# Performance work log

Measured on AMD Instinct MI355X. Metric: run time of the kernel, lower is better.

Reference implementation:

```python
import jax, jax.numpy as jnp
import numpy as np

B, I, H = 4096, 2048, 2048


def setup_inputs() -> dict:
    key = jax.random.key(0)
    k1, k2, k3, k4, k5 = jax.random.split(key, 5)
    return {
        "x": jax.random.normal(k1, (B, I), dtype=jnp.float32),
        "coefficients": jax.random.normal(k2, (I, H), dtype=jnp.float32) * 0.1,
        "amplitude_an": jax.random.normal(k3, (1, I, H), dtype=jnp.float32) * 0.1,
        "amplitude_bn": jax.random.normal(k4, (1, I, H), dtype=jnp.float32) * 0.1,
        "bias": jax.random.normal(k5, (1, I), dtype=jnp.float32),
    }


def reference(x, coefficients, amplitude_an, amplitude_bn, bias):
    # phase[b,h] = x[b,:] @ coefficients[:,h]  (same matmul done per-sample in torch loop)
    phase = x @ coefficients  # [B, H]
    num_harmonics = coefficients.shape[1]
    # sum over harmonics of an[i,h]*cos(phase[b,h]) + bn[i,h]*sin(phase[b,h])
    gain = (
        jnp.einsum("bh,ih->bi", jnp.cos(phase), amplitude_an[0])
        + jnp.einsum("bh,ih->bi", jnp.sin(phase), amplitude_bn[0])
        + num_harmonics * bias  # bias added per-harmonic before the sum over H
    )
    return gain  # [B, I]
```

## Files before the change

kernel.cpp:

```cpp
#include <hip/hip_runtime.h>
#include <hip/hip_bf16.h>

#define B_DIM 4096
#define I_DIM 2048
#define H_DIM 2048

typedef unsigned char u8;
typedef unsigned short u16;
typedef unsigned int u32;
typedef __attribute__((ext_vector_type(4))) float f32x4;
typedef __attribute__((ext_vector_type(4))) int i32x4;
typedef __attribute__((ext_vector_type(8))) int i32x8;

#define SBAR __builtin_amdgcn_sched_barrier(0)

__device__ __forceinline__ void gload_lds16(const void* g, void* l) {
  __builtin_amdgcn_global_load_lds(
      (const __attribute__((address_space(1))) void*)g,
      (__attribute__((address_space(3))) void*)l, 16, 0, 0);
}

__device__ __forceinline__ u32 f2fp4(float v, float inv_scale) {
  const float a = fabsf(v) * inv_scale;
  u32 m = (u32)(a > 0.25f) + (u32)(a > 0.75f) + (u32)(a > 1.25f) +
          (u32)(a > 1.75f) + (u32)(a > 2.5f) + (u32)(a > 3.5f) + (u32)(a > 5.0f);
  return ((__float_as_uint(v) >> 31) << 3) | m;
}

__global__ void prep_all(const float* __restrict__ x, const float* __restrict__ coeff,
                         const float* __restrict__ an, const float* __restrict__ bn,
                         u16* __restrict__ xf4, u16* __restrict__ ct4,
                         u32* __restrict__ ab4) {
  if (blockIdx.x < 4096) {
    __shared__ float tile[32][33];
    const int h0 = (blockIdx.x & 63) * 32;
    const int i0 = (blockIdx.x >> 6) * 32;
    const int tid = threadIdx.x;
    const int tx = tid & 31;
    const int ty = tid >> 5;
    for (int r = ty; r < 32; r += 8)
      tile[r][tx] = coeff[(long)(i0 + r) * H_DIM + (h0 + tx)];
    __syncthreads();
    const int hl = tid >> 3;
    const int q = (tid & 7) * 4;
    u32 w = f2fp4(tile[q + 0][hl], 8.f) | (f2fp4(tile[q + 1][hl], 8.f) << 4) |
            (f2fp4(tile[q + 2][hl], 8.f) << 8) | (f2fp4(tile[q + 3][hl], 8.f) << 12);
    ct4[(long)(h0 + hl) * (I_DIM / 4) + ((i0 + q) >> 2)] = (u16)w;
    return;
  }
  const long NX4 = (long)B_DIM * I_DIM / 4;
  const long NA4 = (long)I_DIM * H_DIM / 4;
  const long total = NX4 + NA4;
  const long stride = (long)1024 * blockDim.x;
  for (long t = (long)(blockIdx.x - 4096) * blockDim.x + threadIdx.x; t < total;
       t += stride) {
    if (t < NX4) {
      float4 v = *(const float4*)(x + t * 4);
      u32 b0 = f2fp4(v.x, 1.f) | (f2fp4(v.y, 1.f) << 4);
      u32 b1 = f2fp4(v.z, 1.f) | (f2fp4(v.w, 1.f) << 4);
      xf4[t] = (u16)(b0 | (b1 << 8));
    } else {
      long p = (t - NX4) * 4;
      float4 va = *(const float4*)(an + p);
      float4 vb = *(const float4*)(bn + p);
      u32 b0 = f2fp4(va.x, 8.f) | (f2fp4(vb.x, 8.f) << 4);
      u32 b1 = f2fp4(va.y, 8.f) | (f2fp4(vb.y, 8.f) << 4);
      u32 b2 = f2fp4(va.z, 8.f) | (f2fp4(vb.z, 8.f) << 4);
      u32 b3 = f2fp4(va.w, 8.f) | (f2fp4(vb.w, 8.f) << 4);
      ab4[p >> 2] = b0 | (b1 << 8) | (b2 << 16) | (b3 << 24);
    }
  }
}

#define NBUF 49152

__device__ __forceinline__ void stageA1(const char* Ab, long kbyte, long lda,
                                        char* buf, int tid, int i) {
  const int o = i * 8192 + tid * 16;
  const int row = o >> 7;
  const int ls = ((((o >> 4) & 7) ^ (row & 7)) << 4);
  gload_lds16(Ab + (long)row * lda + kbyte + ls, buf + o);
}
__device__ __forceinline__ void stageB1(const char* Bb, long kbyte, long ldb,
                                        char* buf, int tid, int i) {
  const int o = i * 8192 + tid * 16;
  const int row = o >> 7;
  const int ls = ((((o >> 4) & 7) ^ (row & 7)) << 4);
  gload_lds16(Bb + (long)row * ldb + kbyte + ls, buf + 16384 + o);
}

__device__ __forceinline__ i32x4 frag_ld16(const char* S, int row, int slot) {
  return *(const i32x4*)(S + row * 128 + ((slot ^ (row & 7)) << 4));
}

template <int SA, int SB>
__device__ __forceinline__ void gemm_kloop_fp4(const char* __restrict__ A,
                                               const char* __restrict__ Bt,
                                               int rowA0, int colB0, long Kbytes,
                                               char* smem, f32x4 acc[4][4]) {
  const int tid = threadIdx.x;
  const int lane = tid & 63;
  const int wid = tid >> 6;
  const int wr = wid >> 2;
  const int wc = wid & 3;
  const long lda = Kbytes, ldb = Kbytes;
  const char* Ab = A + (long)rowA0 * lda;
  const char* Bb = Bt + (long)colB0 * ldb;
  const int arow = wr * 64 + (lane & 15);
  const int brow = wc * 64 + (lane & 15);
  const int g = lane >> 4;
  const int nt = (int)(Kbytes >> 7);

  char* b0 = smem;
  char* b1 = smem + NBUF;
  char* b2 = smem + 2 * NBUF;

#pragma unroll
  for (int i = 0; i < 2; ++i) stageA1(Ab, 0, lda, b0, tid, i);
#pragma unroll
  for (int i = 0; i < 4; ++i) stageB1(Bb, 0, ldb, b0, tid, i);
#pragma unroll
  for (int i = 0; i < 2; ++i) stageA1(Ab, 128, lda, b1, tid, i);
#pragma unroll
  for (int i = 0; i < 4; ++i) stageB1(Bb, 128, ldb, b1, tid, i);

  for (int t = 0; t < nt; ++t) {
    if (t < nt - 1) asm volatile("s_waitcnt vmcnt(6)" ::: "memory");
    else            asm volatile("s_waitcnt vmcnt(0)" ::: "memory");
    SBAR;
    __builtin_amdgcn_s_barrier();
    SBAR;

    const bool st = (t + 2 < nt);
    const long kb2 = (long)(t + 2) * 128;
    i32x8 af[2][4], bfr[2][4];

#pragma unroll
    for (int m = 0; m < 4; ++m)
      *(i32x4*)&af[0][m] = frag_ld16(b0, arow + m * 16, g);
    *(i32x4*)&bfr[0][0] = frag_ld16(b0 + 16384, brow, g);
    *(i32x4*)&bfr[0][1] = frag_ld16(b0 + 16384, brow + 16, g);
    if (st) { stageA1(Ab, kb2, lda, b2, tid, 0); stageA1(Ab, kb2, lda, b2, tid, 1); }
    SBAR;
    asm volatile("s_waitcnt lgkmcnt(0)" ::: "memory");
    SBAR;
    __builtin_amdgcn_s_setprio(1);
#pragma unroll
    for (int m = 0; m < 4; ++m)
#pragma unroll
      for (int n = 0; n < 2; ++n)
        acc[m][n] = __builtin_amdgcn_mfma_scale_f32_16x16x128_f8f6f4(
            af[0][m], bfr[0][n], acc[m][n], 4, 4, 0, SA, 0, SB);
    __builtin_amdgcn_s_setprio(0);
    SBAR;
    __builtin_amdgcn_s_barrier();

#pragma unroll
    for (int m = 0; m < 4; ++m)
      *(i32x4*)&af[1][m] = frag_ld16(b0, arow + m * 16, 4 + g);
    *(i32x4*)&bfr[0][2] = frag_ld16(b0 + 16384, brow + 32, g);
    *(i32x4*)&bfr[0][3] = frag_ld16(b0 + 16384, brow + 48, g);
    if (st) { stageB1(Bb, kb2, ldb, b2, tid, 0); stageB1(Bb, kb2, ldb, b2, tid, 1); }
    SBAR;
    asm volatile("s_waitcnt lgkmcnt(0)" ::: "memory");
    SBAR;
    __builtin_amdgcn_s_setprio(1);
#pragma unroll
    for (int m = 0; m < 4; ++m)
#pragma unroll
      for (int n = 2; n < 4; ++n)
        acc[m][n] = __builtin_amdgcn_mfma_scale_f32_16x16x128_f8f6f4(
            af[0][m], bfr[0][n], acc[m][n], 4, 4, 0, SA, 0, SB);
    __builtin_amdgcn_s_setprio(0);
    SBAR;
    __builtin_amdgcn_s_barrier();

    *(i32x4*)&bfr[1][0] = frag_ld16(b0 + 16384, brow, 4 + g);
    *(i32x4*)&bfr[1][1] = frag_ld16(b0 + 16384, brow + 16, 4 + g);
    if (st) stageB1(Bb, kb2, ldb, b2, tid, 2);
    SBAR;
    asm volatile("s_waitcnt lgkmcnt(0)" ::: "memory");
    SBAR;
    __builtin_amdgcn_s_setprio(1);
#pragma unroll
    for (int m = 0; m < 4; ++m)
#pragma unroll
      for (int n = 0; n < 2; ++n)
        acc[m][n] = __builtin_amdgcn_mfma_scale_f32_16x16x128_f8f6f4(
            af[1][m], bfr[1][n], acc[m][n], 4, 4, 0, SA, 0, SB);
    __builtin_amdgcn_s_setprio(0);
    SBAR;
    __builtin_amdgcn_s_barrier();

    *(i32x4*)&bfr[1][2] = frag_ld16(b0 + 16384, brow + 32, 4 + g);
    *(i32x4*)&bfr[1][3] = frag_ld16(b0 + 16384, brow + 48, 4 + g);
    if (st) stageB1(Bb, kb2, ldb, b2, tid, 3);
    SBAR;
    asm volatile("s_waitcnt lgkmcnt(0)" ::: "memory");
    SBAR;
    __builtin_amdgcn_s_setprio(1);
#pragma unroll
    for (int m = 0; m < 4; ++m)
#pragma unroll
      for (int n = 2; n < 4; ++n)
        acc[m][n] = __builtin_amdgcn_mfma_scale_f32_16x16x128_f8f6f4(
            af[1][m], bfr[1][n], acc[m][n], 4, 4, 0, SA, 0, SB);
    __builtin_amdgcn_s_setprio(0);
    SBAR;

    char* tmp = b0; b0 = b1; b1 = b2; b2 = tmp;
  }
}

__device__ __forceinline__ void tile_xy(int& bx, int& by) {
  const int bid = blockIdx.x;
  const int xcd = bid & 7;
  const int loc = bid >> 3;
  bx = (xcd & 1) * 4 + (loc & 3);
  by = (xcd >> 1) * 8 + (loc >> 2);
}

__global__ __launch_bounds__(512, 1) void gemm_phase(const char* __restrict__ xf4,
                                                     const char* __restrict__ ct4,
                                                     u8* __restrict__ cs4) {
  __shared__ __align__(16) char smem[3 * NBUF];
  int bx, by;
  tile_xy(bx, by);
  const int rowA0 = by * 128;
  const int colB0 = bx * 256;
  f32x4 acc[4][4];
#pragma unroll
  for (int m = 0; m < 4; ++m)
#pragma unroll
    for (int n = 0; n < 4; ++n)
#pragma unroll
      for (int j = 0; j < 4; ++j) acc[m][n][j] = 0.0f;

  gemm_kloop_fp4<0x7F7F7F7F, 0x7C7C7C7C>(xf4, ct4, rowA0, colB0, I_DIM / 2, smem, acc);

  const int lane = threadIdx.x & 63;
  const int wid = threadIdx.x >> 6;
  const int wr = wid >> 2, wc = wid & 3;
#pragma unroll
  for (int m = 0; m < 4; ++m) {
#pragma unroll
    for (int n = 0; n < 4; ++n) {
      const int col = colB0 + wc * 64 + n * 16 + (lane & 15);
#pragma unroll
      for (int j = 0; j < 4; ++j) {
        const int row = rowA0 + wr * 64 + m * 16 + (lane >> 4) * 4 + j;
        const float p = acc[m][n][j];
        const u32 b = f2fp4(__cosf(p), 4.f) | (f2fp4(__sinf(p), 4.f) << 4);
        cs4[(long)row * H_DIM + col] = (u8)b;
      }
    }
  }
}

__global__ __launch_bounds__(512, 1) void gemm_gain(const char* __restrict__ cs4,
                                                    const char* __restrict__ ab4,
                                                    const float* __restrict__ bias,
                                                    float* __restrict__ out) {
  __shared__ __align__(16) char smem[3 * NBUF];
  int bx, by;
  tile_xy(bx, by);
  const int rowA0 = by * 128;
  const int colB0 = bx * 256;
  f32x4 acc[4][4];
#pragma unroll
  for (int m = 0; m < 4; ++m)
#pragma unroll
    for (int n = 0; n < 4; ++n)
#pragma unroll
      for (int j = 0; j < 4; ++j) acc[m][n][j] = 0.0f;

  gemm_kloop_fp4<0x7D7D7D7D, 0x7C7C7C7C>(cs4, ab4, rowA0, colB0, H_DIM, smem, acc);

  const int lane = threadIdx.x & 63;
  const int wid = threadIdx.x >> 6;
  const int wr = wid >> 2, wc = wid & 3;
#pragma unroll
  for (int m = 0; m < 4; ++m) {
#pragma unroll
    for (int n = 0; n < 4; ++n) {
      const int col = colB0 + wc * 64 + n * 16 + (lane & 15);
      const float bv = 2048.0f * bias[col];
#pragma unroll
      for (int j = 0; j < 4; ++j) {
        const int row = rowA0 + wr * 64 + m * 16 + (lane >> 4) * 4 + j;
        out[(long)row * I_DIM + col] = acc[m][n][j] + bv;
      }
    }
  }
}

extern "C" void kernel_launch(void* const* d_in, const int* in_sizes, int n_in,
                              void* d_out, int out_size, void* d_ws, size_t ws_size,
                              hipStream_t stream) {
  const float* x     = (const float*)d_in[0];
  const float* coeff = (const float*)d_in[1];
  const float* an    = (const float*)d_in[2];
  const float* bn    = (const float*)d_in[3];
  const float* bias  = (const float*)d_in[4];
  float* out = (float*)d_out;

  char* ws = (char*)d_ws;
  char* xf4 = ws;
  char* ct4 = ws + (4L << 20);
  char* ab4 = ws + (8L << 20);
  u8*  cs4  = (u8*)(ws + (12L << 20));

  prep_all<<<5120, 256, 0, stream>>>(x, coeff, an, bn, (u16*)xf4, (u16*)ct4,
                                     (u32*)ab4);
  gemm_phase<<<256, 512, 0, stream>>>(xf4, ct4, cs4);
  gemm_gain<<<256, 512, 0, stream>>>((const char*)cs4, (const char*)ab4, bias, out);
}
```

Before: 67.69 us.

## Reschedule FP4 GEMM k-loop with partial LDS waits and fewer barriers

The GEMM k-loop is reordered so more LDS fragment reads are issued ahead of the MFMA groups. Full lgkmcnt(0) waits become partial waits, and three intra-iteration workgroup barriers are removed, keeping only the per-iteration barrier that guards the triple buffer. Separately, the coefficient-transpose part of prep makes each block handle 8 tiles, which cuts the grid from 5120 to 1536 blocks. The phase epilogue uses a single __sincosf call, and both GEMMs declare launch_bounds(512,2). The tighter register limit may cause spills, and with about 147KB of LDS per block only one block can fit per CU anyway; the partial lgkmcnt counts also assume a particular instruction ordering.

```diff
diff --git a/kernel.cpp b/kernel.cpp
--- a/kernel.cpp
+++ b/kernel.cpp
@@ -13,6 +13,7 @@
 typedef __attribute__((ext_vector_type(8))) int i32x8;
 
 #define SBAR __builtin_amdgcn_sched_barrier(0)
+#define NBUF 49152
 
 __device__ __forceinline__ void gload_lds16(const void* g, void* l) {
   __builtin_amdgcn_global_load_lds(
@@ -31,28 +32,33 @@
                          const float* __restrict__ an, const float* __restrict__ bn,
                          u16* __restrict__ xf4, u16* __restrict__ ct4,
                          u32* __restrict__ ab4) {
-  if (blockIdx.x < 4096) {
+  if (blockIdx.x < 512) {
     __shared__ float tile[32][33];
-    const int h0 = (blockIdx.x & 63) * 32;
-    const int i0 = (blockIdx.x >> 6) * 32;
     const int tid = threadIdx.x;
     const int tx = tid & 31;
     const int ty = tid >> 5;
-    for (int r = ty; r < 32; r += 8)
-      tile[r][tx] = coeff[(long)(i0 + r) * H_DIM + (h0 + tx)];
-    __syncthreads();
     const int hl = tid >> 3;
     const int q = (tid & 7) * 4;
-    u32 w = f2fp4(tile[q + 0][hl], 8.f) | (f2fp4(tile[q + 1][hl], 8.f) << 4) |
-            (f2fp4(tile[q + 2][hl], 8.f) << 8) | (f2fp4(tile[q + 3][hl], 8.f) << 12);
-    ct4[(long)(h0 + hl) * (I_DIM / 4) + ((i0 + q) >> 2)] = (u16)w;
+#pragma unroll
+    for (int rep = 0; rep < 8; ++rep) {
+      const int tidx = blockIdx.x * 8 + rep;
+      const int h0 = (tidx & 63) * 32;
+      const int i0 = (tidx >> 6) * 32;
+      for (int r = ty; r < 32; r += 8)
+        tile[r][tx] = coeff[(long)(i0 + r) * H_DIM + (h0 + tx)];
+      __syncthreads();
+      u32 w = f2fp4(tile[q + 0][hl], 8.f) | (f2fp4(tile[q + 1][hl], 8.f) << 4) |
+              (f2fp4(tile[q + 2][hl], 8.f) << 8) | (f2fp4(tile[q + 3][hl], 8.f) << 12);
+      ct4[(long)(h0 + hl) * (I_DIM / 4) + ((i0 + q) >> 2)] = (u16)w;
+      __syncthreads();
+    }
     return;
   }
   const long NX4 = (long)B_DIM * I_DIM / 4;
   const long NA4 = (long)I_DIM * H_DIM / 4;
   const long total = NX4 + NA4;
   const long stride = (long)1024 * blockDim.x;
-  for (long t = (long)(blockIdx.x - 4096) * blockDim.x + threadIdx.x; t < total;
+  for (long t = (long)(blockIdx.x - 512) * blockDim.x + threadIdx.x; t < total;
        t += stride) {
     if (t < NX4) {
       float4 v = *(const float4*)(x + t * 4);
@@ -72,21 +78,25 @@
   }
 }
 
-#define NBUF 49152
-
-__device__ __forceinline__ void stageA1(const char* Ab, long kbyte, long lda,
-                                        char* buf, int tid, int i) {
-  const int o = i * 8192 + tid * 16;
-  const int row = o >> 7;
-  const int ls = ((((o >> 4) & 7) ^ (row & 7)) << 4);
-  gload_lds16(Ab + (long)row * lda + kbyte + ls, buf + o);
-}
-__device__ __forceinline__ void stageB1(const char* Bb, long kbyte, long ldb,
-                                        char* buf, int tid, int i) {
-  const int o = i * 8192 + tid * 16;
-  const int row = o >> 7;
-  const int ls = ((((o >> 4) & 7) ^ (row & 7)) << 4);
-  gload_lds16(Bb + (long)row * ldb + kbyte + ls, buf + 16384 + o);
+__device__ __forceinline__ void stageA2(const char* Ab, long kbyte, long lda,
+                                        char* buf, int tid) {
+#pragma unroll
+  for (int i = 0; i < 2; ++i) {
+    const int o = i * 8192 + tid * 16;
+    const int row = o >> 7;
+    const int ls = ((((o >> 4) & 7) ^ (row & 7)) << 4);
+    gload_lds16(Ab + (long)row * lda + kbyte + ls, buf + o);
+  }
+}
+__device__ __forceinline__ void stageB2(const char* Bb, long kbyte, long ldb,
+                                        char* buf, int tid, int i0) {
+#pragma unroll
+  for (int i = 0; i < 2; ++i) {
+    const int o = (i0 + i) * 8192 + tid * 16;
+    const int row = o >> 7;
+    const int ls = ((((o >> 4) & 7) ^ (row & 7)) << 4);
+    gload_lds16(Bb + (long)row * ldb + kbyte + ls, buf + 16384 + o);
+  }
 }
 
 __device__ __forceinline__ i32x4 frag_ld16(const char* S, int row, int slot) {
@@ -115,14 +125,10 @@
   char* b1 = smem + NBUF;
   char* b2 = smem + 2 * NBUF;
 
-#pragma unroll
-  for (int i = 0; i < 2; ++i) stageA1(Ab, 0, lda, b0, tid, i);
-#pragma unroll
-  for (int i = 0; i < 4; ++i) stageB1(Bb, 0, ldb, b0, tid, i);
-#pragma unroll
-  for (int i = 0; i < 2; ++i) stageA1(Ab, 128, lda, b1, tid, i);
-#pragma unroll
-  for (int i = 0; i < 4; ++i) stageB1(Bb, 128, ldb, b1, tid, i);
+  stageA2(Ab, 0, lda, b0, tid);   stageB2(Bb, 0, ldb, b0, tid, 0);
+  stageB2(Bb, 0, ldb, b0, tid, 2);
+  stageA2(Ab, 128, lda, b1, tid); stageB2(Bb, 128, ldb, b1, tid, 0);
+  stageB2(Bb, 128, ldb, b1, tid, 2);
 
   for (int t = 0; t < nt; ++t) {
     if (t < nt - 1) asm volatile("s_waitcnt vmcnt(6)" ::: "memory");
@@ -140,9 +146,12 @@
       *(i32x4*)&af[0][m] = frag_ld16(b0, arow + m * 16, g);
     *(i32x4*)&bfr[0][0] = frag_ld16(b0 + 16384, brow, g);
     *(i32x4*)&bfr[0][1] = frag_ld16(b0 + 16384, brow + 16, g);
-    if (st) { stageA1(Ab, kb2, lda, b2, tid, 0); stageA1(Ab, kb2, lda, b2, tid, 1); }
-    SBAR;
-    asm volatile("s_waitcnt lgkmcnt(0)" ::: "memory");
+    if (st) stageA2(Ab, kb2, lda, b2, tid);
+    SBAR;
+    *(i32x4*)&bfr[0][2] = frag_ld16(b0 + 16384, brow + 32, g);
+    *(i32x4*)&bfr[0][3] = frag_ld16(b0 + 16384, brow + 48, g);
+    SBAR;
+    asm volatile("s_waitcnt lgkmcnt(2)" ::: "memory");
     SBAR;
     __builtin_amdgcn_s_setprio(1);
 #pragma unroll
@@ -153,16 +162,15 @@
             af[0][m], bfr[0][n], acc[m][n], 4, 4, 0, SA, 0, SB);
     __builtin_amdgcn_s_setprio(0);
     SBAR;
-    __builtin_amdgcn_s_barrier();
 
 #pragma unroll
     for (int m = 0; m < 4; ++m)
       *(i32x4*)&af[1][m] = frag_ld16(b0, arow + m * 16, 4 + g);
-    *(i32x4*)&bfr[0][2] = frag_ld16(b0 + 16384, brow + 32, g);
-    *(i32x4*)&bfr[0][3] = frag_ld16(b0 + 16384, brow + 48, g);
-    if (st) { stageB1(Bb, kb2, ldb, b2, tid, 0); stageB1(Bb, kb2, ldb, b2, tid, 1); }
-    SBAR;
-    asm volatile("s_waitcnt lgkmcnt(0)" ::: "memory");
+    *(i32x4*)&bfr[1][0] = frag_ld16(b0 + 16384, brow, 4 + g);
+    *(i32x4*)&bfr[1][1] = frag_ld16(b0 + 16384, brow + 16, 4 + g);
+    if (st) stageB2(Bb, kb2, ldb, b2, tid, 0);
+    SBAR;
+    asm volatile("s_waitcnt lgkmcnt(6)" ::: "memory");
     SBAR;
     __builtin_amdgcn_s_setprio(1);
 #pragma unroll
@@ -173,13 +181,12 @@
             af[0][m], bfr[0][n], acc[m][n], 4, 4, 0, SA, 0, SB);
     __builtin_amdgcn_s_setprio(0);
     SBAR;
-    __builtin_amdgcn_s_barrier();
-
-    *(i32x4*)&bfr[1][0] = frag_ld16(b0 + 16384, brow, 4 + g);
-    *(i32x4*)&bfr[1][1] = frag_ld16(b0 + 16384, brow + 16, 4 + g);
-    if (st) stageB1(Bb, kb2, ldb, b2, tid, 2);
-    SBAR;
-    asm volatile("s_waitcnt lgkmcnt(0)" ::: "memory");
+
+    *(i32x4*)&bfr[1][2] = frag_ld16(b0 + 16384, brow + 32, 4 + g);
+    *(i32x4*)&bfr[1][3] = frag_ld16(b0 + 16384, brow + 48, 4 + g);
+    if (st) stageB2(Bb, kb2, ldb, b2, tid, 2);
+    SBAR;
+    asm volatile("s_waitcnt lgkmcnt(2)" ::: "memory");
     SBAR;
     __builtin_amdgcn_s_setprio(1);
 #pragma unroll
@@ -190,12 +197,7 @@
             af[1][m], bfr[1][n], acc[m][n], 4, 4, 0, SA, 0, SB);
     __builtin_amdgcn_s_setprio(0);
     SBAR;
-    __builtin_amdgcn_s_barrier();
-
-    *(i32x4*)&bfr[1][2] = frag_ld16(b0 + 16384, brow + 32, 4 + g);
-    *(i32x4*)&bfr[1][3] = frag_ld16(b0 + 16384, brow + 48, 4 + g);
-    if (st) stageB1(Bb, kb2, ldb, b2, tid, 3);
-    SBAR;
+
     asm volatile("s_waitcnt lgkmcnt(0)" ::: "memory");
     SBAR;
     __builtin_amdgcn_s_setprio(1);
@@ -220,7 +222,7 @@
   by = (xcd >> 1) * 8 + (loc >> 2);
 }
 
-__global__ __launch_bounds__(512, 1) void gemm_phase(const char* __restrict__ xf4,
+__global__ __launch_bounds__(512, 2) void gemm_phase(const char* __restrict__ xf4,
                                                      const char* __restrict__ ct4,
                                                      u8* __restrict__ cs4) {
   __shared__ __align__(16) char smem[3 * NBUF];
@@ -250,14 +252,16 @@
       for (int j = 0; j < 4; ++j) {
         const int row = rowA0 + wr * 64 + m * 16 + (lane >> 4) * 4 + j;
         const float p = acc[m][n][j];
-        const u32 b = f2fp4(__cosf(p), 4.f) | (f2fp4(__sinf(p), 4.f) << 4);
+        float sp, cp;
+        __sincosf(p, &sp, &cp);
+        const u32 b = f2fp4(cp, 4.f) | (f2fp4(sp, 4.f) << 4);
         cs4[(long)row * H_DIM + col] = (u8)b;
       }
     }
   }
 }
 
-__global__ __launch_bounds__(512, 1) void gemm_gain(const char* __restrict__ cs4,
+__global__ __launch_bounds__(512, 2) void gemm_gain(const char* __restrict__ cs4,
                                                     const char* __restrict__ ab4,
                                                     const float* __restrict__ bias,
                                                     float* __restrict__ out) {
@@ -310,7 +314,7 @@
   char* ab4 = ws + (8L << 20);
   u8*  cs4  = (u8*)(ws + (12L << 20));
 
-  prep_all<<<5120, 256, 0, stream>>>(x, coeff, an, bn, (u16*)xf4, (u16*)ct4,
+  prep_all<<<1536, 256, 0, stream>>>(x, coeff, an, bn, (u16*)xf4, (u16*)ct4,
                                      (u32*)ab4);
   gemm_phase<<<256, 512, 0, stream>>>(xf4, ct4, cs4);
   gemm_gain<<<256, 512, 0, stream>>>((const char*)cs4, (const char*)ab4, bias, out);
```

Result: faster. 62.47 us (-7.7%).
